# Kernel optimization log

Measured on AMD Instinct MI355X. Metric: run time of the kernel, lower is better.

## Reference

```python
import jax, jax.numpy as jnp
import numpy as np

B, Q, S, H, D = 4, 1024, 2048, 32, 128  # batch, new tokens, cache capacity, heads, head_dim
SCALE = 0.08838834764831845  # 1/sqrt(128)


def setup_inputs() -> dict:
    key = jax.random.key(0)
    ks = jax.random.split(key, 7)
    query_states = jax.random.normal(ks[0], (B, Q, H, D), jnp.float32)
    key_states = jax.random.normal(ks[1], (B, Q, H, D), jnp.float32)
    value_states = jax.random.normal(ks[2], (B, Q, H, D), jnp.float32)
    k_cache = jax.random.normal(ks[3], (B, S, H, D), jnp.float32)
    v_cache = jax.random.normal(ks[4], (B, S, H, D), jnp.float32)
    q_lens = jax.random.randint(ks[5], (B,), 1, Q + 1).astype(jnp.int32)      # ragged new lengths
    cache_lens = jax.random.randint(ks[6], (B,), 0, Q + 1).astype(jnp.int32)  # prior context lengths
    return dict(query_states=query_states, key_states=key_states, value_states=value_states,
                k_cache=k_cache, v_cache=v_cache, q_lens=q_lens, cache_lens=cache_lens)


def _update_cache(cache, new, cache_lens, q_lens):
    # Per-sequence append: write new[b, :q_len[b]] into cache[b, cache_len[b]:cache_len[b]+q_len[b]]
    def upd(c, n, clen, qlen):
        j = jnp.arange(Q)
        idx = jnp.clip(clen + j, 0, S - 1)               # [Q]
        valid = j < qlen                                  # [Q]
        vals = jnp.where(valid[:, None, None], n, c[idx])  # keep old value where padded
        return c.at[idx].set(vals)
    return jax.vmap(upd)(cache, new, cache_lens, q_lens)


def reference(query_states, key_states, value_states, k_cache, v_cache, q_lens, cache_lens):
    kc = _update_cache(k_cache, key_states, cache_lens, q_lens)   # [B,S,H,D]
    vc = _update_cache(v_cache, value_states, cache_lens, q_lens)

    scores = jnp.einsum('bqhd,bkhd->bhqk', query_states, kc) * SCALE  # [B,H,Q,S]

    qi = jnp.arange(Q)
    kj = jnp.arange(S)
    # query i may attend to cache pos j iff j < cache_len + min(i+1, q_len)  (causal + segment bound)
    limit = cache_lens[:, None] + jnp.minimum(qi[None, :] + 1, q_lens[:, None])  # [B,Q]
    mask = kj[None, None, :] < limit[:, :, None]                                  # [B,Q,S]
    scores = jnp.where(mask[:, None, :, :], scores, -jnp.inf)
    probs = jax.nn.softmax(scores, axis=-1)

    out = jnp.einsum('bhqk,bkhd->bqhd', probs, vc)  # [B,Q,H,D]
    q_valid = (qi[None, :] < q_lens[:, None])[:, :, None, None]
    return jnp.where(q_valid, out, jnp.zeros((), out.dtype))
```

## Files before the change

kernel.cpp:

```cpp
#include <hip/hip_runtime.h>


#define BB 4
#define QQ 1024
#define SS 2048
#define HH 32
#define DD 128
#define QT 64
#define KT 32
#define NTILES 64
#define TILE_ELEMS 4096
#define NPERQ 256

typedef __attribute__((ext_vector_type(8))) short short8;
typedef __attribute__((ext_vector_type(4))) float f32x4;
typedef __attribute__((ext_vector_type(16))) float f32x16;
typedef __attribute__((ext_vector_type(4))) unsigned int u32x4;
typedef __attribute__((ext_vector_type(8))) unsigned short u16x8;

__device__ __forceinline__ unsigned short f2bf(float f) {
    unsigned int u = __builtin_bit_cast(unsigned int, f);
    u += 0x7FFFu + ((u >> 16) & 1u);
    return (unsigned short)(u >> 16);
}
__device__ __forceinline__ unsigned int cvtpk(float lo, float hi) {
    unsigned int r;
    asm("v_cvt_pk_bf16_f32 %0, %1, %2" : "=v"(r) : "v"(lo), "v"(hi));
    return r;
}
__device__ __forceinline__ void glds16(const unsigned short* g, unsigned short* l) {
    __builtin_amdgcn_global_load_lds(
        (const __attribute__((address_space(1))) unsigned int*)g,
        (__attribute__((address_space(3))) unsigned int*)l, 16, 0, 0);
}

__global__ __launch_bounds__(256)
void prep(const float* __restrict__ ks, const float* __restrict__ vs,
          const float* __restrict__ kc_, const float* __restrict__ vc,
          const int* __restrict__ qlens, const int* __restrict__ clens,
          unsigned short* __restrict__ Kws, unsigned short* __restrict__ Vws)
{
    const int tile = blockIdx.x, h = blockIdx.y, b = blockIdx.z;
    const int qlen = qlens[b], clen = clens[b];
    if (tile * KT >= clen + qlen) return;
    const int tid = threadIdx.x;
    unsigned short* kout = Kws + (((size_t)b * HH + h) * NTILES + tile) * TILE_ELEMS;
    unsigned short* vout = Vws + (((size_t)b * HH + h) * NTILES + tile) * TILE_ELEMS;

    #pragma unroll
    for (int h2 = 0; h2 < 2; ++h2) {
        const int idx8 = h2 * 2048 + tid * 8;
        const int c = idx8 >> 9, l = (idx8 >> 3) & 63;
        int key = tile * KT + (l & 31);
        const float* src;
        if (key < clen) {
            src = kc_ + (((size_t)b * SS + key) * HH + h) * DD;
        } else {
            int i2 = key - clen; if (i2 > QQ - 1) i2 = QQ - 1;
            src = ks + (((size_t)b * QQ + i2) * HH + h) * DD;
        }
        const int d0 = c * 16 + ((l >> 5) << 3);
        f32x4 a0 = *(const f32x4*)&src[d0];
        f32x4 a1 = *(const f32x4*)&src[d0 + 4];
        u16x8 w;
        w[0] = f2bf(a0[0]); w[1] = f2bf(a0[1]); w[2] = f2bf(a0[2]); w[3] = f2bf(a0[3]);
        w[4] = f2bf(a1[0]); w[5] = f2bf(a1[1]); w[6] = f2bf(a1[2]); w[7] = f2bf(a1[3]);
        *(u16x8*)&kout[idx8] = w;
    }
    #pragma unroll
    for (int h2 = 0; h2 < 2; ++h2) {
        const int idx8 = h2 * 2048 + tid * 8;
        const int a = idx8 >> 9, l = (idx8 >> 3) & 63;
        const int dchunk = a >> 1, kcc = a & 1;
        const int d = dchunk * 32 + (l & 31);
        const int kb = tile * KT + kcc * 16 + ((l >> 5) << 3);
        u16x8 w;
        #pragma unroll
        for (int e = 0; e < 8; ++e) {
            int key = kb + e;
            const float* src;
            if (key < clen) {
                src = vc + (((size_t)b * SS + key) * HH + h) * DD;
            } else {
                int i2 = key - clen; if (i2 > QQ - 1) i2 = QQ - 1;
                src = vs + (((size_t)b * QQ + i2) * HH + h) * DD;
            }
            w[e] = f2bf(src[d]);
        }
        *(u16x8*)&vout[idx8] = w;
    }
}

#define TSTEP(T, SC, SN, BC, BN)                                                \
{                                                                               \
    const int pbase = (T) * KT;                                                 \
    if (pbase + KT > lim_min) {                                                 \
        _Pragma("unroll")                                                       \
        for (int r = 0; r < 16; ++r) {                                          \
            const int kk = pbase + (r & 3) + ((r >> 2) << 3) + hi * 4;          \
            if (kk >= lim_l) SC[r] = -3e38f;                                    \
        }                                                                       \
    }                                                                           \
    float pm = fmaxf(fmaxf(fmaxf(fmaxf(SC[0], SC[1]), fmaxf(SC[2], SC[3])),     \
                           fmaxf(fmaxf(SC[4], SC[5]), fmaxf(SC[6], SC[7]))),    \
                     fmaxf(fmaxf(fmaxf(SC[8], SC[9]), fmaxf(SC[10], SC[11])),   \
                           fmaxf(fmaxf(SC[12], SC[13]), fmaxf(SC[14], SC[15])))); \
    if (__any(pm > m_ + 8.0f)) {                                                \
        pm = fmaxf(pm, __shfl_xor(pm, 32));                                     \
        const float mn = fmaxf(m_, pm);                                         \
        const float alpha = __builtin_amdgcn_exp2f(m_ - mn);                    \
        m_ = mn;                                                                \
        l_ *= alpha;                                                            \
        _Pragma("unroll")                                                       \
        for (int r = 0; r < 16; ++r) {                                          \
            o0[r] *= alpha; o1[r] *= alpha; o2[r] *= alpha; o3[r] *= alpha;     \
        }                                                                       \
    }                                                                           \
    float p[16];                                                                \
    _Pragma("unroll")                                                           \
    for (int r = 0; r < 16; ++r) p[r] = __builtin_amdgcn_exp2f(SC[r] - m_);     \
    l_ += (((p[0]+p[1])+(p[2]+p[3])) + ((p[4]+p[5])+(p[6]+p[7])))               \
        + (((p[8]+p[9])+(p[10]+p[11])) + ((p[12]+p[13])+(p[14]+p[15])));        \
    const unsigned int w0 = cvtpk(p[0],  p[1]);                                 \
    const unsigned int w1 = cvtpk(p[2],  p[3]);                                 \
    const unsigned int w2 = cvtpk(p[4],  p[5]);                                 \
    const unsigned int w3 = cvtpk(p[6],  p[7]);                                 \
    const unsigned int w4 = cvtpk(p[8],  p[9]);                                 \
    const unsigned int w5 = cvtpk(p[10], p[11]);                                \
    const unsigned int w6 = cvtpk(p[12], p[13]);                                \
    const unsigned int w7 = cvtpk(p[14], p[15]);                                \
    const unsigned int x0 = (unsigned int)__shfl_xor((int)w0, 32);              \
    const unsigned int x1 = (unsigned int)__shfl_xor((int)w1, 32);              \
    const unsigned int x2 = (unsigned int)__shfl_xor((int)w2, 32);              \
    const unsigned int x3 = (unsigned int)__shfl_xor((int)w3, 32);              \
    const unsigned int x4 = (unsigned int)__shfl_xor((int)w4, 32);              \
    const unsigned int x5 = (unsigned int)__shfl_xor((int)w5, 32);              \
    const unsigned int x6 = (unsigned int)__shfl_xor((int)w6, 32);              \
    const unsigned int x7 = (unsigned int)__shfl_xor((int)w7, 32);              \
    u32x4 pb0w, pb1w;                                                           \
    pb0w[0] = hiL ? x2 : w0;  pb0w[1] = hiL ? x3 : w1;                          \
    pb0w[2] = hiL ? w2 : x0;  pb0w[3] = hiL ? w3 : x1;                          \
    pb1w[0] = hiL ? x6 : w4;  pb1w[1] = hiL ? x7 : w5;                          \
    pb1w[2] = hiL ? w6 : x4;  pb1w[3] = hiL ? w7 : x5;                          \
    const short8 pb0 = __builtin_bit_cast(short8, pb0w);                        \
    const short8 pb1 = __builtin_bit_cast(short8, pb1w);                        \
    asm volatile("s_waitcnt vmcnt(0)" ::: "memory");                            \
    __builtin_amdgcn_s_barrier();                                               \
    __builtin_amdgcn_sched_barrier(0);                                          \
    SN = (f32x16){0.f};                                                         \
    __builtin_amdgcn_s_setprio(1);                                              \
    _Pragma("unroll")                                                           \
    for (int c = 0; c < 8; ++c) {                                               \
        short8 kf = *(const short8*)&KVl[BN][c * 512 + lane * 8];               \
        SN = __builtin_amdgcn_mfma_f32_32x32x16_bf16(kf, qf[c], SN, 0, 0, 0);   \
    }                                                                           \
    {                                                                           \
        short8 va = *(const short8*)&KVl[BC][4096 + 0 * 512 + lane * 8];        \
        short8 vb = *(const short8*)&KVl[BC][4096 + 1 * 512 + lane * 8];        \
        o0 = __builtin_amdgcn_mfma_f32_32x32x16_bf16(va, pb0, o0, 0, 0, 0);     \
        o0 = __builtin_amdgcn_mfma_f32_32x32x16_bf16(vb, pb1, o0, 0, 0, 0);     \
    }                                                                           \
    {                                                                           \
        short8 va = *(const short8*)&KVl[BC][4096 + 2 * 512 + lane * 8];        \
        short8 vb = *(const short8*)&KVl[BC][4096 + 3 * 512 + lane * 8];        \
        o1 = __builtin_amdgcn_mfma_f32_32x32x16_bf16(va, pb0, o1, 0, 0, 0);     \
        o1 = __builtin_amdgcn_mfma_f32_32x32x16_bf16(vb, pb1, o1, 0, 0, 0);     \
    }                                                                           \
    {                                                                           \
        short8 va = *(const short8*)&KVl[BC][4096 + 4 * 512 + lane * 8];        \
        short8 vb = *(const short8*)&KVl[BC][4096 + 5 * 512 + lane * 8];        \
        o2 = __builtin_amdgcn_mfma_f32_32x32x16_bf16(va, pb0, o2, 0, 0, 0);     \
        o2 = __builtin_amdgcn_mfma_f32_32x32x16_bf16(vb, pb1, o2, 0, 0, 0);     \
    }                                                                           \
    {                                                                           \
        short8 va = *(const short8*)&KVl[BC][4096 + 6 * 512 + lane * 8];        \
        short8 vb = *(const short8*)&KVl[BC][4096 + 7 * 512 + lane * 8];        \
        o3 = __builtin_amdgcn_mfma_f32_32x32x16_bf16(va, pb0, o3, 0, 0, 0);     \
        o3 = __builtin_amdgcn_mfma_f32_32x32x16_bf16(vb, pb1, o3, 0, 0, 0);     \
    }                                                                           \
    __builtin_amdgcn_s_setprio(0);                                              \
    asm volatile("s_waitcnt lgkmcnt(0)" ::: "memory");                          \
    __builtin_amdgcn_s_barrier();                                               \
    __builtin_amdgcn_sched_barrier(0);                                          \
    const int t2c = ((T) + 2 < nt) ? (T) + 2 : (nt - 1);                        \
    const unsigned short* k2p = Kb + (size_t)t2c * TILE_ELEMS;                  \
    const unsigned short* v2p = Vb + (size_t)t2c * TILE_ELEMS;                  \
    _Pragma("unroll")                                                           \
    for (int j = 0; j < 4; ++j) {                                               \
        glds16(&k2p[sbase + j * 512], &KVl[BC][lbase + j * 512]);               \
        glds16(&v2p[sbase + j * 512], &KVl[BC][4096 + lbase + j * 512]);        \
    }                                                                           \
}

__global__ __launch_bounds__(128, 2)
void segattn_persist(const float* __restrict__ qs, const int* __restrict__ qlens,
                     const int* __restrict__ clens,
                     const unsigned short* __restrict__ Kws,
                     const unsigned short* __restrict__ Vws,
                     float* __restrict__ out, int* __restrict__ counter)
{
    __shared__ int s_item;
    alignas(16) __shared__ unsigned short KVl[2][8192];

    const int tid = threadIdx.x, w = tid >> 6, lane = tid & 63;
    const int q31 = lane & 31, hi = lane >> 5;
    const bool hiL = (hi != 0);
    const float psc = 0.08838834764831845f * 1.4426950408889634f;
    const int sbase = w * 2048 + lane * 8;
    const int lbase = w * 2048;
    const int cres = blockIdx.x & 7;
    int* myctr = counter + cres;

    for (;;) {
        if (tid == 0) s_item = atomicAdd(myctr, 1);
        __syncthreads();
        const int pop = s_item;
        __syncthreads();
        if (pop >= NPERQ) break;

        const int bhi = pop >> 4, qtord = pop & 15;
        const int qt = 15 - qtord;
        const int b = bhi & 3, h = cres + 8 * (bhi >> 2);
        const int qlen = qlens[b], clen = clens[b];
        const int q0 = qt * QT;

        if (q0 >= qlen) {
            f32x4 z = {0.f, 0.f, 0.f, 0.f};
            #pragma unroll
            for (int i2 = 0; i2 < 16; ++i2) {
                int f = tid + i2 * 128;
                int r = f >> 5, d4 = f & 31;
                *(f32x4*)&out[(((size_t)b * QQ + q0 + r) * HH + h) * DD + d4 * 4] = z;
            }
            continue;
        }

        const int q = q0 + w * 32 + q31;
        const float* qp = qs + (((size_t)b * QQ + q) * HH + h) * DD;
        short8 qf[8];
        #pragma unroll
        for (int c = 0; c < 8; ++c) {
            const int d0 = c * 16 + hi * 8;
            f32x4 a0 = *(const f32x4*)&qp[d0];
            f32x4 a1 = *(const f32x4*)&qp[d0 + 4];
            short8 t;
            t[0] = (short)f2bf(a0[0] * psc); t[1] = (short)f2bf(a0[1] * psc);
            t[2] = (short)f2bf(a0[2] * psc); t[3] = (short)f2bf(a0[3] * psc);
            t[4] = (short)f2bf(a1[0] * psc); t[5] = (short)f2bf(a1[1] * psc);
            t[6] = (short)f2bf(a1[2] * psc); t[7] = (short)f2bf(a1[3] * psc);
            qf[c] = t;
        }

        const int lim_l = (q < qlen) ? (clen + q + 1) : 0;
        const int wq0 = q0 + w * 32;
        const int lim_min = (wq0 + 31 < qlen) ? (clen + wq0 + 1) : 0;

        float m_ = -3e38f, l_ = 0.f;
        f32x16 o0 = {0}, o1 = {0}, o2 = {0}, o3 = {0};

        const int kmax = clen + min(q0 + QT, qlen);
        const int nt = (kmax + KT - 1) / KT;
        const unsigned short* Kb = Kws + ((size_t)(b * HH + h)) * NTILES * TILE_ELEMS;
        const unsigned short* Vb = Vws + ((size_t)(b * HH + h)) * NTILES * TILE_ELEMS;

        #pragma unroll
        for (int j = 0; j < 4; ++j) {
            glds16(&Kb[sbase + j * 512], &KVl[0][lbase + j * 512]);
            glds16(&Vb[sbase + j * 512], &KVl[0][4096 + lbase + j * 512]);
        }
        asm volatile("s_waitcnt vmcnt(0)" ::: "memory");
        __builtin_amdgcn_s_barrier();
        __builtin_amdgcn_sched_barrier(0);
        {
            const int t1x = (nt > 1) ? 1 : 0;
            const unsigned short* k1p = Kb + (size_t)t1x * TILE_ELEMS;
            const unsigned short* v1p = Vb + (size_t)t1x * TILE_ELEMS;
            #pragma unroll
            for (int j = 0; j < 4; ++j) {
                glds16(&k1p[sbase + j * 512], &KVl[1][lbase + j * 512]);
                glds16(&v1p[sbase + j * 512], &KVl[1][4096 + lbase + j * 512]);
            }
        }
        f32x16 sA = {0}, sB;
        __builtin_amdgcn_s_setprio(1);
        #pragma unroll
        for (int c = 0; c < 8; ++c) {
            short8 kf = *(const short8*)&KVl[0][c * 512 + lane * 8];
            sA = __builtin_amdgcn_mfma_f32_32x32x16_bf16(kf, qf[c], sA, 0, 0, 0);
        }
        __builtin_amdgcn_s_setprio(0);

        int t = 0;
        for (; t + 2 <= nt; t += 2) {
            TSTEP(t,     sA, sB, 0, 1);
            TSTEP(t + 1, sB, sA, 1, 0);
        }
        if (t < nt) {
            TSTEP(t, sA, sB, 0, 1);
        }

        float lt = l_ + __shfl_xor(l_, 32);
        const bool val = (q < qlen);
        const float inv = val ? (1.0f / lt) : 0.f;
        float* op = out + (((size_t)b * QQ + q) * HH + h) * DD;
        #pragma unroll
        for (int rr = 0; rr < 4; ++rr) {
            f32x4 wv;
            const int d0 = rr * 8 + hi * 4;
            wv[0] = o0[rr*4+0]*inv; wv[1] = o0[rr*4+1]*inv;
            wv[2] = o0[rr*4+2]*inv; wv[3] = o0[rr*4+3]*inv;
            *(f32x4*)&op[d0] = wv;
            wv[0] = o1[rr*4+0]*inv; wv[1] = o1[rr*4+1]*inv;
            wv[2] = o1[rr*4+2]*inv; wv[3] = o1[rr*4+3]*inv;
            *(f32x4*)&op[32 + d0] = wv;
            wv[0] = o2[rr*4+0]*inv; wv[1] = o2[rr*4+1]*inv;
            wv[2] = o2[rr*4+2]*inv; wv[3] = o2[rr*4+3]*inv;
            *(f32x4*)&op[64 + d0] = wv;
            wv[0] = o3[rr*4+0]*inv; wv[1] = o3[rr*4+1]*inv;
            wv[2] = o3[rr*4+2]*inv; wv[3] = o3[rr*4+3]*inv;
            *(f32x4*)&op[96 + d0] = wv;
        }
    }
}

__global__ __launch_bounds__(256)
void segattn(const float* __restrict__ qs, const float* __restrict__ ks,
             const float* __restrict__ vs, const float* __restrict__ kc,
             const float* __restrict__ vc, const int* __restrict__ qlens,
             const int* __restrict__ clens, float* __restrict__ out)
{
    const int qt = blockIdx.x, h = blockIdx.y, b = blockIdx.z;
    const int tid = threadIdx.x, wave = tid >> 6, lane = tid & 63;
    const int g = lane >> 4, lc = lane & 15;
    const int qlen = qlens[b], clen = clens[b];
    const int q0 = qt * QT;
    if (q0 >= qlen) {
        f32x4 z = {0.f, 0.f, 0.f, 0.f};
        #pragma unroll
        for (int i2 = 0; i2 < 8; ++i2) {
            int f = tid + i2 * 256;
            int r = f >> 5, d4 = f & 31;
            *(f32x4*)&out[(((size_t)b * QQ + q0 + r) * HH + h) * DD + d4 * 4] = z;
        }
        return;
    }
    alignas(16) __shared__ unsigned short Kl[KT * DD];
    alignas(16) __shared__ unsigned short Vl[DD * 40];
    alignas(16) __shared__ unsigned short Pl[4][16][40];
    const float psc = 0.08838834764831845f * 1.4426950408889634f;
    const int qrow = q0 + wave * 16 + lc;
    const float* qp = qs + (((size_t)b * QQ + qrow) * HH + h) * DD;
    short8 qf[4];
    #pragma unroll
    for (int c = 0; c < 4; ++c) {
        f32x4 a0 = *(const f32x4*)&qp[c * 32 + g * 8];
        f32x4 a1 = *(const f32x4*)&qp[c * 32 + g * 8 + 4];
        short8 t;
        t[0] = (short)f2bf(a0[0] * psc); t[1] = (short)f2bf(a0[1] * psc);
        t[2] = (short)f2bf(a0[2] * psc); t[3] = (short)f2bf(a0[3] * psc);
        t[4] = (short)f2bf(a1[0] * psc); t[5] = (short)f2bf(a1[1] * psc);
        t[6] = (short)f2bf(a1[2] * psc); t[7] = (short)f2bf(a1[3] * psc);
        qf[c] = t;
    }
    f32x4 o[8];
    #pragma unroll
    for (int n = 0; n < 8; ++n) o[n] = (f32x4){0.f, 0.f, 0.f, 0.f};
    float m_[4] = {-3e38f, -3e38f, -3e38f, -3e38f};
    float l_[4] = {0.f, 0.f, 0.f, 0.f};
    int lim[4];
    #pragma unroll
    for (int qq = 0; qq < 4; ++qq) {
        int i = q0 + wave * 16 + g * 4 + qq;
        lim[qq] = (i < qlen) ? (clen + i + 1) : 0;
    }
    const int kmax = clen + min(q0 + QT, qlen);
    const int nt = (kmax + KT - 1) / KT;
    for (int t = 0; t < nt; ++t) {
        const int pbase = t * KT;
        __syncthreads();
        #pragma unroll
        for (int it = 0; it < 4; ++it) {
            int f = tid + it * 256;
            int key = f >> 5, d4 = f & 31;
            int p = pbase + key;
            const float *srck, *srcv;
            if (p < clen) {
                size_t off = (((size_t)b * SS + p) * HH + h) * DD + d4 * 4;
                srck = kc + off; srcv = vc + off;
            } else {
                int idx = p - clen; if (idx > QQ - 1) idx = QQ - 1;
                size_t off = (((size_t)b * QQ + idx) * HH + h) * DD + d4 * 4;
                srck = ks + off; srcv = vs + off;
            }
            f32x4 kv = *(const f32x4*)srck;
            f32x4 vv = *(const f32x4*)srcv;
            int ei = (key * DD + d4 * 4) ^ ((key & 7) << 3);
            typedef __attribute__((ext_vector_type(4))) unsigned short u16x4;
            u16x4 kb4 = {f2bf(kv[0]), f2bf(kv[1]), f2bf(kv[2]), f2bf(kv[3])};
            *(u16x4*)&Kl[ei] = kb4;
            int d0 = d4 * 4;
            Vl[(d0 + 0) * 40 + key] = f2bf(vv[0]);
            Vl[(d0 + 1) * 40 + key] = f2bf(vv[1]);
            Vl[(d0 + 2) * 40 + key] = f2bf(vv[2]);
            Vl[(d0 + 3) * 40 + key] = f2bf(vv[3]);
        }
        __syncthreads();
        f32x4 sc0 = {0.f, 0.f, 0.f, 0.f}, sc1 = {0.f, 0.f, 0.f, 0.f};
        #pragma unroll
        for (int c = 0; c < 4; ++c) {
            int i0 = (lc * DD + c * 32 + g * 8) ^ ((lc & 7) << 3);
            int i1 = ((16 + lc) * DD + c * 32 + g * 8) ^ (((16 + lc) & 7) << 3);
            short8 k0 = *(const short8*)&Kl[i0];
            short8 k1 = *(const short8*)&Kl[i1];
            sc0 = __builtin_amdgcn_mfma_f32_16x16x32_bf16(qf[c], k0, sc0, 0, 0, 0);
            sc1 = __builtin_amdgcn_mfma_f32_16x16x32_bf16(qf[c], k1, sc1, 0, 0, 0);
        }
        float pr0[4], pr1[4];
        #pragma unroll
        for (int qq = 0; qq < 4; ++qq) {
            float s0 = sc0[qq], s1 = sc1[qq];
            if (pbase + lc >= lim[qq])      s0 = -3e38f;
            if (pbase + 16 + lc >= lim[qq]) s1 = -3e38f;
            float pm = fmaxf(s0, s1);
            #pragma unroll
            for (int d2 = 1; d2 < 16; d2 <<= 1) pm = fmaxf(pm, __shfl_xor(pm, d2));
            float mn = fmaxf(m_[qq], pm);
            float alpha = exp2f(m_[qq] - mn);
            float p0 = exp2f(s0 - mn), p1 = exp2f(s1 - mn);
            float rs = p0 + p1;
            #pragma unroll
            for (int d2 = 1; d2 < 16; d2 <<= 1) rs += __shfl_xor(rs, d2);
            l_[qq] = l_[qq] * alpha + rs;
            m_[qq] = mn;
            pr0[qq] = p0; pr1[qq] = p1;
            #pragma unroll
            for (int n = 0; n < 8; ++n) o[n][qq] *= alpha;
        }
        #pragma unroll
        for (int qq = 0; qq < 4; ++qq) {
            Pl[wave][g * 4 + qq][lc]      = f2bf(pr0[qq]);
            Pl[wave][g * 4 + qq][16 + lc] = f2bf(pr1[qq]);
        }
        short8 pf = *(const short8*)&Pl[wave][lc][g * 8];
        #pragma unroll
        for (int n = 0; n < 8; ++n) {
            short8 vf = *(const short8*)&Vl[(n * 16 + lc) * 40 + g * 8];
            o[n] = __builtin_amdgcn_mfma_f32_16x16x32_bf16(pf, vf, o[n], 0, 0, 0);
        }
    }
    #pragma unroll
    for (int qq = 0; qq < 4; ++qq) {
        int i = q0 + wave * 16 + g * 4 + qq;
        bool val = (i < qlen);
        float inv = val ? (1.0f / l_[qq]) : 0.f;
        size_t ob = (((size_t)b * QQ + i) * HH + h) * DD + lc;
        #pragma unroll
        for (int n = 0; n < 8; ++n)
            out[ob + (size_t)n * 16] = val ? o[n][qq] * inv : 0.f;
    }
}

extern "C" void kernel_launch(void* const* d_in, const int* in_sizes, int n_in,
                              void* d_out, int out_size, void* d_ws, size_t ws_size,
                              hipStream_t stream) {
    const float* qs = (const float*)d_in[0];
    const float* ks = (const float*)d_in[1];
    const float* vs = (const float*)d_in[2];
    const float* kc = (const float*)d_in[3];
    const float* vc = (const float*)d_in[4];
    const int* ql = (const int*)d_in[5];
    const int* cl = (const int*)d_in[6];
    float* o = (float*)d_out;

    const size_t kv_elems = (size_t)BB * HH * NTILES * TILE_ELEMS;
    const size_t kv_bytes = kv_elems * 2 * sizeof(unsigned short);
    const size_t need = kv_bytes + 128;

    if (ws_size >= need) {
        unsigned short* Kws = (unsigned short*)d_ws;
        unsigned short* Vws = Kws + kv_elems;
        int* counter = (int*)((char*)d_ws + kv_bytes);
        hipMemsetAsync(counter, 0, 128, stream);
        dim3 pgrid(NTILES, HH, BB), pblk(256, 1, 1);
        hipLaunchKernelGGL(prep, pgrid, pblk, 0, stream, ks, vs, kc, vc, ql, cl, Kws, Vws);
        dim3 grid(1024, 1, 1), blk(128, 1, 1);
        hipLaunchKernelGGL(segattn_persist, grid, blk, 0, stream, qs, ql, cl, Kws, Vws, o, counter);
    } else {
        dim3 grid(QQ / QT, HH, BB), blk(256, 1, 1);
        hipLaunchKernelGGL(segattn, grid, blk, 0, stream, qs, ks, vs, kc, vc, ql, cl, o);
    }
}
```

Before: 156.5 us.

## Double persistent attention query tile to 128 rows with four-wave blocks

The persistent kernel now handles 128 query rows per work item with 256-thread (four-wave) blocks instead of 64 rows with two waves. Each K/V tile staged in shared memory is reused by twice as many queries, and the load work per tile is split across four waves. Clamping and store guards are added for rows past the sequence end. The costs are coarser causal tiles, so more masked work at the diagonal, fewer work items for load balancing, and one block per CU under the new launch bounds.

```diff
diff --git a/kernel.cpp b/kernel.cpp
--- a/kernel.cpp
+++ b/kernel.cpp
@@ -6,11 +6,10 @@
 #define SS 2048
 #define HH 32
 #define DD 128
-#define QT 64
 #define KT 32
 #define NTILES 64
 #define TILE_ELEMS 4096
-#define NPERQ 256
+#define NPERQ 128
 
 typedef __attribute__((ext_vector_type(8))) short short8;
 typedef __attribute__((ext_vector_type(4))) float f32x4;
@@ -186,13 +185,13 @@
     const unsigned short* k2p = Kb + (size_t)t2c * TILE_ELEMS;                  \
     const unsigned short* v2p = Vb + (size_t)t2c * TILE_ELEMS;                  \
     _Pragma("unroll")                                                           \
-    for (int j = 0; j < 4; ++j) {                                               \
-        glds16(&k2p[sbase + j * 512], &KVl[BC][lbase + j * 512]);               \
-        glds16(&v2p[sbase + j * 512], &KVl[BC][4096 + lbase + j * 512]);        \
-    }                                                                           \
-}
-
-__global__ __launch_bounds__(128, 2)
+    for (int j = 0; j < 2; ++j) {                                               \
+        glds16(&k2p[gsl + j * 512], &KVl[BC][lsl + j * 512]);                   \
+        glds16(&v2p[gsl + j * 512], &KVl[BC][4096 + lsl + j * 512]);            \
+    }                                                                           \
+}
+
+__global__ __launch_bounds__(256, 1)
 void segattn_persist(const float* __restrict__ qs, const int* __restrict__ qlens,
                      const int* __restrict__ clens,
                      const unsigned short* __restrict__ Kws,
@@ -206,8 +205,8 @@
     const int q31 = lane & 31, hi = lane >> 5;
     const bool hiL = (hi != 0);
     const float psc = 0.08838834764831845f * 1.4426950408889634f;
-    const int sbase = w * 2048 + lane * 8;
-    const int lbase = w * 2048;
+    const int gsl = w * 1024 + lane * 8;
+    const int lsl = w * 1024;
     const int cres = blockIdx.x & 7;
     int* myctr = counter + cres;
 
@@ -218,17 +217,16 @@
         __syncthreads();
         if (pop >= NPERQ) break;
 
-        const int bhi = pop >> 4, qtord = pop & 15;
-        const int qt = 15 - qtord;
+        const int bhi = pop >> 3, jt = 7 - (pop & 7);
         const int b = bhi & 3, h = cres + 8 * (bhi >> 2);
         const int qlen = qlens[b], clen = clens[b];
-        const int q0 = qt * QT;
+        const int q0 = jt * 128;
 
         if (q0 >= qlen) {
             f32x4 z = {0.f, 0.f, 0.f, 0.f};
             #pragma unroll
             for (int i2 = 0; i2 < 16; ++i2) {
-                int f = tid + i2 * 128;
+                int f = tid + i2 * 256;
                 int r = f >> 5, d4 = f & 31;
                 *(f32x4*)&out[(((size_t)b * QQ + q0 + r) * HH + h) * DD + d4 * 4] = z;
             }
@@ -236,7 +234,8 @@
         }
 
         const int q = q0 + w * 32 + q31;
-        const float* qp = qs + (((size_t)b * QQ + q) * HH + h) * DD;
+        const int qcl = (q < QQ) ? q : (QQ - 1);
+        const float* qp = qs + (((size_t)b * QQ + qcl) * HH + h) * DD;
         short8 qf[8];
         #pragma unroll
         for (int c = 0; c < 8; ++c) {
@@ -258,15 +257,15 @@
         float m_ = -3e38f, l_ = 0.f;
         f32x16 o0 = {0}, o1 = {0}, o2 = {0}, o3 = {0};
 
-        const int kmax = clen + min(q0 + QT, qlen);
+        const int kmax = clen + min(q0 + 128, qlen);
         const int nt = (kmax + KT - 1) / KT;
         const unsigned short* Kb = Kws + ((size_t)(b * HH + h)) * NTILES * TILE_ELEMS;
         const unsigned short* Vb = Vws + ((size_t)(b * HH + h)) * NTILES * TILE_ELEMS;
 
         #pragma unroll
-        for (int j = 0; j < 4; ++j) {
-            glds16(&Kb[sbase + j * 512], &KVl[0][lbase + j * 512]);
-            glds16(&Vb[sbase + j * 512], &KVl[0][4096 + lbase + j * 512]);
+        for (int j = 0; j < 2; ++j) {
+            glds16(&Kb[gsl + j * 512], &KVl[0][lsl + j * 512]);
+            glds16(&Vb[gsl + j * 512], &KVl[0][4096 + lsl + j * 512]);
         }
         asm volatile("s_waitcnt vmcnt(0)" ::: "memory");
         __builtin_amdgcn_s_barrier();
@@ -276,9 +275,9 @@
             const unsigned short* k1p = Kb + (size_t)t1x * TILE_ELEMS;
             const unsigned short* v1p = Vb + (size_t)t1x * TILE_ELEMS;
             #pragma unroll
-            for (int j = 0; j < 4; ++j) {
-                glds16(&k1p[sbase + j * 512], &KVl[1][lbase + j * 512]);
-                glds16(&v1p[sbase + j * 512], &KVl[1][4096 + lbase + j * 512]);
+            for (int j = 0; j < 2; ++j) {
+                glds16(&k1p[gsl + j * 512], &KVl[1][lsl + j * 512]);
+                glds16(&v1p[gsl + j * 512], &KVl[1][4096 + lsl + j * 512]);
             }
         }
         f32x16 sA = {0}, sB;
@@ -302,23 +301,23 @@
         float lt = l_ + __shfl_xor(l_, 32);
         const bool val = (q < qlen);
         const float inv = val ? (1.0f / lt) : 0.f;
-        float* op = out + (((size_t)b * QQ + q) * HH + h) * DD;
+        float* op = out + (((size_t)b * QQ + qcl) * HH + h) * DD;
         #pragma unroll
         for (int rr = 0; rr < 4; ++rr) {
             f32x4 wv;
             const int d0 = rr * 8 + hi * 4;
             wv[0] = o0[rr*4+0]*inv; wv[1] = o0[rr*4+1]*inv;
             wv[2] = o0[rr*4+2]*inv; wv[3] = o0[rr*4+3]*inv;
-            *(f32x4*)&op[d0] = wv;
+            if (val || q < QQ) *(f32x4*)&op[d0] = wv;
             wv[0] = o1[rr*4+0]*inv; wv[1] = o1[rr*4+1]*inv;
             wv[2] = o1[rr*4+2]*inv; wv[3] = o1[rr*4+3]*inv;
-            *(f32x4*)&op[32 + d0] = wv;
+            if (val || q < QQ) *(f32x4*)&op[32 + d0] = wv;
             wv[0] = o2[rr*4+0]*inv; wv[1] = o2[rr*4+1]*inv;
             wv[2] = o2[rr*4+2]*inv; wv[3] = o2[rr*4+3]*inv;
-            *(f32x4*)&op[64 + d0] = wv;
+            if (val || q < QQ) *(f32x4*)&op[64 + d0] = wv;
             wv[0] = o3[rr*4+0]*inv; wv[1] = o3[rr*4+1]*inv;
             wv[2] = o3[rr*4+2]*inv; wv[3] = o3[rr*4+3]*inv;
-            *(f32x4*)&op[96 + d0] = wv;
+            if (val || q < QQ) *(f32x4*)&op[96 + d0] = wv;
         }
     }
 }
@@ -333,7 +332,7 @@
     const int tid = threadIdx.x, wave = tid >> 6, lane = tid & 63;
     const int g = lane >> 4, lc = lane & 15;
     const int qlen = qlens[b], clen = clens[b];
-    const int q0 = qt * QT;
+    const int q0 = qt * 64;
     if (q0 >= qlen) {
         f32x4 z = {0.f, 0.f, 0.f, 0.f};
         #pragma unroll
@@ -373,7 +372,7 @@
         int i = q0 + wave * 16 + g * 4 + qq;
         lim[qq] = (i < qlen) ? (clen + i + 1) : 0;
     }
-    const int kmax = clen + min(q0 + QT, qlen);
+    const int kmax = clen + min(q0 + 64, qlen);
     const int nt = (kmax + KT - 1) / KT;
     for (int t = 0; t < nt; ++t) {
         const int pbase = t * KT;
@@ -483,10 +482,10 @@
         hipMemsetAsync(counter, 0, 128, stream);
         dim3 pgrid(NTILES, HH, BB), pblk(256, 1, 1);
         hipLaunchKernelGGL(prep, pgrid, pblk, 0, stream, ks, vs, kc, vc, ql, cl, Kws, Vws);
-        dim3 grid(1024, 1, 1), blk(128, 1, 1);
+        dim3 grid(512, 1, 1), blk(256, 1, 1);
         hipLaunchKernelGGL(segattn_persist, grid, blk, 0, stream, qs, ql, cl, Kws, Vws, o, counter);
     } else {
-        dim3 grid(QQ / QT, HH, BB), blk(256, 1, 1);
+        dim3 grid(QQ / 64, HH, BB), blk(256, 1, 1);
         hipLaunchKernelGGL(segattn, grid, blk, 0, stream, qs, ks, vs, kc, vc, ql, cl, o);
     }
 }
```

Measured after the change: 178.0 us. +13.8%, slower.
